# Performance work log

Measured on AMD Instinct MI355X. Metric: run time of the kernel, lower is better.

## Reference

```python
import jax, jax.numpy as jnp
import numpy as np

N_FRAMES = 20000
N_BEADS = 50


def _feature_indices(n_beads):
    # cgnet's get_distance_indices ordering: by pair separation, then start index
    dist = np.array([(i, i + inc) for inc in range(1, n_beads)
                     for i in range(n_beads - inc)], dtype=np.int32)
    ang = np.array([(i, i + 1, i + 2) for i in range(n_beads - 2)], dtype=np.int32)
    dih = np.array([(i, i + 1, i + 2, i + 3) for i in range(n_beads - 3)], dtype=np.int32)
    return dist, ang, dih


def setup_inputs() -> dict:
    key = jax.random.key(0)
    data = jax.random.normal(key, (N_FRAMES, N_BEADS, 3), dtype=jnp.float32) * 3.0
    return {"data": data}


def reference(data):
    # data: [n_frames, n_beads, 3]
    n_beads = data.shape[1]
    dist_inds, ang_inds, dih_inds = _feature_indices(n_beads)

    # --- pairwise distances: ||x_j - x_i|| -> [F, n_dist]
    dvec = data[:, dist_inds[:, 1]] - data[:, dist_inds[:, 0]]
    distances = jnp.linalg.norm(dvec, axis=-1)

    # --- planar angles at middle bead j of (i, j, k) -> [F, n_ang]
    b1 = data[:, ang_inds[:, 0]] - data[:, ang_inds[:, 1]]
    b2 = data[:, ang_inds[:, 2]] - data[:, ang_inds[:, 1]]
    cos_theta = jnp.sum(b1 * b2, axis=-1) / (
        jnp.linalg.norm(b1, axis=-1) * jnp.linalg.norm(b2, axis=-1))
    angles = jnp.arccos(jnp.clip(cos_theta, -1.0, 1.0))

    # --- dihedrals of (i, j, k, l): cross-product plane normals -> cos, sin
    a = data[:, dih_inds[:, 1]] - data[:, dih_inds[:, 0]]
    b = data[:, dih_inds[:, 2]] - data[:, dih_inds[:, 1]]
    c = data[:, dih_inds[:, 3]] - data[:, dih_inds[:, 2]]
    p1 = jnp.cross(a, b)          # normal of plane (i,j,k)
    p2 = jnp.cross(b, c)          # normal of plane (j,k,l)
    n1 = jnp.linalg.norm(p1, axis=-1)
    n2 = jnp.linalg.norm(p2, axis=-1)
    dih_cos = jnp.sum(p1 * p2, axis=-1) / (n1 * n2)
    dih_sin = jnp.sum(jnp.cross(p1, p2) * b, axis=-1) / (
        n1 * n2 * jnp.linalg.norm(b, axis=-1))

    # description_order: Distances, Angles, Dihedral_cosines, Dihedral_sines
    return jnp.concatenate([distances, angles, dih_cos, dih_sin], axis=1)
```

## Files before the change

kernel.cpp:

```cpp
#include <hip/hip_runtime.h>
#include <math.h>

#define N_FRAMES 20000
#define N_BEADS  50
#define N_DIST   1225
#define N_ANG    48
#define N_DIH    47
#define OUT_STRIDE (N_DIST + N_ANG + 2 * N_DIH)

__device__ __forceinline__ int cum_pairs(int inc) {
    return (inc - 1) * 50 - ((inc - 1) * inc) / 2;
}

__global__ __launch_bounds__(256)
void protein_feat_kernel(const float* __restrict__ data, float* __restrict__ out) {
    const int f   = blockIdx.x;
    const int tid = threadIdx.x;

    __shared__ float s[N_BEADS * 3];

    const float* fd = data + (size_t)f * (N_BEADS * 3);
    if (tid < N_BEADS * 3) s[tid] = fd[tid];
    __syncthreads();

    float* fout = out + (size_t)f * OUT_STRIDE;

    for (int p = tid; p < N_DIST; p += 256) {
        float disc = 9801.0f - 8.0f * (float)p;
        int inc = (int)((101.0f - sqrtf(disc)) * 0.5f);
        inc = min(max(inc, 1), 49);
        while (inc < 49 && cum_pairs(inc + 1) <= p) ++inc;
        while (inc > 1  && cum_pairs(inc)     >  p) --inc;
        int i = p - cum_pairs(inc);
        int j = i + inc;

        float dx = s[3 * j + 0] - s[3 * i + 0];
        float dy = s[3 * j + 1] - s[3 * i + 1];
        float dz = s[3 * j + 2] - s[3 * i + 2];
        fout[p] = sqrtf(dx * dx + dy * dy + dz * dz);
    }

    if (tid < N_ANG) {
        int a = tid;
        float b1x = s[3 * a + 0] - s[3 * (a + 1) + 0];
        float b1y = s[3 * a + 1] - s[3 * (a + 1) + 1];
        float b1z = s[3 * a + 2] - s[3 * (a + 1) + 2];
        float b2x = s[3 * (a + 2) + 0] - s[3 * (a + 1) + 0];
        float b2y = s[3 * (a + 2) + 1] - s[3 * (a + 1) + 1];
        float b2z = s[3 * (a + 2) + 2] - s[3 * (a + 1) + 2];
        float dot = b1x * b2x + b1y * b2y + b1z * b2z;
        float n1 = sqrtf(b1x * b1x + b1y * b1y + b1z * b1z);
        float n2 = sqrtf(b2x * b2x + b2y * b2y + b2z * b2z);
        float c = dot / (n1 * n2);
        c = fminf(1.0f, fmaxf(-1.0f, c));
        fout[N_DIST + a] = acosf(c);
    }

    if (tid >= 64 && tid < 64 + N_DIH) {
        int d = tid - 64;
        float ax = s[3 * (d + 1) + 0] - s[3 * d + 0];
        float ay = s[3 * (d + 1) + 1] - s[3 * d + 1];
        float az = s[3 * (d + 1) + 2] - s[3 * d + 2];
        float bx = s[3 * (d + 2) + 0] - s[3 * (d + 1) + 0];
        float by = s[3 * (d + 2) + 1] - s[3 * (d + 1) + 1];
        float bz = s[3 * (d + 2) + 2] - s[3 * (d + 1) + 2];
        float cx = s[3 * (d + 3) + 0] - s[3 * (d + 2) + 0];
        float cy = s[3 * (d + 3) + 1] - s[3 * (d + 2) + 1];
        float cz = s[3 * (d + 3) + 2] - s[3 * (d + 2) + 2];

        float p1x = ay * bz - az * by;
        float p1y = az * bx - ax * bz;
        float p1z = ax * by - ay * bx;
        float p2x = by * cz - bz * cy;
        float p2y = bz * cx - bx * cz;
        float p2z = bx * cy - by * cx;

        float n1 = sqrtf(p1x * p1x + p1y * p1y + p1z * p1z);
        float n2 = sqrtf(p2x * p2x + p2y * p2y + p2z * p2z);
        float nb = sqrtf(bx * bx + by * by + bz * bz);

        float dotp = p1x * p2x + p1y * p2y + p1z * p2z;
        float qx = p1y * p2z - p1z * p2y;
        float qy = p1z * p2x - p1x * p2z;
        float qz = p1x * p2y - p1y * p2x;
        float trip = qx * bx + qy * by + qz * bz;

        float inv12 = 1.0f / (n1 * n2);
        fout[N_DIST + N_ANG + d]          = dotp * inv12;
        fout[N_DIST + N_ANG + N_DIH + d]  = trip * inv12 / nb;
    }
}

extern "C" void kernel_launch(void* const* d_in, const int* in_sizes, int n_in,
                              void* d_out, int out_size, void* d_ws, size_t ws_size,
                              hipStream_t stream) {
    const float* data = (const float*)d_in[0];
    float* out = (float*)d_out;
    protein_feat_kernel<<<N_FRAMES, 256, 0, stream>>>(data, out);
}
```

Before: 149.2 us.

## Process eight frames per block and reuse pair index decoding across frames

Each block now handles eight frames instead of one. It loads all eight with float4 copies into shared memory and decodes the distance pair indices once into registers, then reuses them for every frame. Angle and dihedral work is spread over all threads across the eight frames rather than leaving most threads idle. This cuts per-block launch and setup overhead and the repeated sqrt-based index search, at the cost of fewer blocks (2500) and more registers per thread.

```diff
diff --git a/kernel.cpp b/kernel.cpp
--- a/kernel.cpp
+++ b/kernel.cpp
@@ -7,6 +7,8 @@
 #define N_ANG    48
 #define N_DIH    47
 #define OUT_STRIDE (N_DIST + N_ANG + 2 * N_DIH)
+#define FPB      8
+#define FRAME_F  (N_BEADS * 3)
 
 __device__ __forceinline__ int cum_pairs(int inc) {
     return (inc - 1) * 50 - ((inc - 1) * inc) / 2;
@@ -14,59 +16,83 @@
 
 __global__ __launch_bounds__(256)
 void protein_feat_kernel(const float* __restrict__ data, float* __restrict__ out) {
-    const int f   = blockIdx.x;
     const int tid = threadIdx.x;
+    const int f0  = blockIdx.x * FPB;
 
-    __shared__ float s[N_BEADS * 3];
+    __shared__ __align__(16) float s[FPB * FRAME_F];
 
-    const float* fd = data + (size_t)f * (N_BEADS * 3);
-    if (tid < N_BEADS * 3) s[tid] = fd[tid];
+    {
+        const float4* g4 = (const float4*)(data + (size_t)f0 * FRAME_F);
+        float4* s4 = (float4*)s;
+        for (int x = tid; x < FPB * FRAME_F / 4; x += 256) s4[x] = g4[x];
+    }
     __syncthreads();
 
-    float* fout = out + (size_t)f * OUT_STRIDE;
-
-    for (int p = tid; p < N_DIST; p += 256) {
-        float disc = 9801.0f - 8.0f * (float)p;
-        int inc = (int)((101.0f - sqrtf(disc)) * 0.5f);
-        inc = min(max(inc, 1), 49);
-        while (inc < 49 && cum_pairs(inc + 1) <= p) ++inc;
-        while (inc > 1  && cum_pairs(inc)     >  p) --inc;
-        int i = p - cum_pairs(inc);
-        int j = i + inc;
-
-        float dx = s[3 * j + 0] - s[3 * i + 0];
-        float dy = s[3 * j + 1] - s[3 * i + 1];
-        float dz = s[3 * j + 2] - s[3 * i + 2];
-        fout[p] = sqrtf(dx * dx + dy * dy + dz * dz);
+    int i3[5], j3[5];
+#pragma unroll
+    for (int k = 0; k < 5; ++k) {
+        int p = tid + k * 256;
+        if (p < N_DIST) {
+            float disc = 9801.0f - 8.0f * (float)p;
+            int inc = (int)((101.0f - sqrtf(disc)) * 0.5f);
+            inc = min(max(inc, 1), 49);
+            while (inc < 49 && cum_pairs(inc + 1) <= p) ++inc;
+            while (inc > 1  && cum_pairs(inc)     >  p) --inc;
+            int i = p - cum_pairs(inc);
+            i3[k] = 3 * i;
+            j3[k] = 3 * (i + inc);
+        } else {
+            i3[k] = 0; j3[k] = 0;
+        }
     }
 
-    if (tid < N_ANG) {
-        int a = tid;
-        float b1x = s[3 * a + 0] - s[3 * (a + 1) + 0];
-        float b1y = s[3 * a + 1] - s[3 * (a + 1) + 1];
-        float b1z = s[3 * a + 2] - s[3 * (a + 1) + 2];
-        float b2x = s[3 * (a + 2) + 0] - s[3 * (a + 1) + 0];
-        float b2y = s[3 * (a + 2) + 1] - s[3 * (a + 1) + 1];
-        float b2z = s[3 * (a + 2) + 2] - s[3 * (a + 1) + 2];
+#pragma unroll
+    for (int f = 0; f < FPB; ++f) {
+        const float* sf = s + f * FRAME_F;
+        float* fout = out + (size_t)(f0 + f) * OUT_STRIDE;
+#pragma unroll
+        for (int k = 0; k < 5; ++k) {
+            int p = tid + k * 256;
+            if (p < N_DIST) {
+                float dx = sf[j3[k] + 0] - sf[i3[k] + 0];
+                float dy = sf[j3[k] + 1] - sf[i3[k] + 1];
+                float dz = sf[j3[k] + 2] - sf[i3[k] + 2];
+                fout[p] = sqrtf(dx * dx + dy * dy + dz * dz);
+            }
+        }
+    }
+
+    for (int idx = tid; idx < FPB * N_ANG; idx += 256) {
+        int f = idx / N_ANG;
+        int a = idx - f * N_ANG;
+        const float* sf = s + f * FRAME_F;
+        float b1x = sf[3 * a + 0] - sf[3 * (a + 1) + 0];
+        float b1y = sf[3 * a + 1] - sf[3 * (a + 1) + 1];
+        float b1z = sf[3 * a + 2] - sf[3 * (a + 1) + 2];
+        float b2x = sf[3 * (a + 2) + 0] - sf[3 * (a + 1) + 0];
+        float b2y = sf[3 * (a + 2) + 1] - sf[3 * (a + 1) + 1];
+        float b2z = sf[3 * (a + 2) + 2] - sf[3 * (a + 1) + 2];
         float dot = b1x * b2x + b1y * b2y + b1z * b2z;
         float n1 = sqrtf(b1x * b1x + b1y * b1y + b1z * b1z);
         float n2 = sqrtf(b2x * b2x + b2y * b2y + b2z * b2z);
         float c = dot / (n1 * n2);
         c = fminf(1.0f, fmaxf(-1.0f, c));
-        fout[N_DIST + a] = acosf(c);
+        out[(size_t)(f0 + f) * OUT_STRIDE + N_DIST + a] = acosf(c);
     }
 
-    if (tid >= 64 && tid < 64 + N_DIH) {
-        int d = tid - 64;
-        float ax = s[3 * (d + 1) + 0] - s[3 * d + 0];
-        float ay = s[3 * (d + 1) + 1] - s[3 * d + 1];
-        float az = s[3 * (d + 1) + 2] - s[3 * d + 2];
-        float bx = s[3 * (d + 2) + 0] - s[3 * (d + 1) + 0];
-        float by = s[3 * (d + 2) + 1] - s[3 * (d + 1) + 1];
-        float bz = s[3 * (d + 2) + 2] - s[3 * (d + 1) + 2];
-        float cx = s[3 * (d + 3) + 0] - s[3 * (d + 2) + 0];
-        float cy = s[3 * (d + 3) + 1] - s[3 * (d + 2) + 1];
-        float cz = s[3 * (d + 3) + 2] - s[3 * (d + 2) + 2];
+    for (int idx = tid; idx < FPB * N_DIH; idx += 256) {
+        int f = idx / N_DIH;
+        int d = idx - f * N_DIH;
+        const float* sf = s + f * FRAME_F;
+        float ax = sf[3 * (d + 1) + 0] - sf[3 * d + 0];
+        float ay = sf[3 * (d + 1) + 1] - sf[3 * d + 1];
+        float az = sf[3 * (d + 1) + 2] - sf[3 * d + 2];
+        float bx = sf[3 * (d + 2) + 0] - sf[3 * (d + 1) + 0];
+        float by = sf[3 * (d + 2) + 1] - sf[3 * (d + 1) + 1];
+        float bz = sf[3 * (d + 2) + 2] - sf[3 * (d + 1) + 2];
+        float cx = sf[3 * (d + 3) + 0] - sf[3 * (d + 2) + 0];
+        float cy = sf[3 * (d + 3) + 1] - sf[3 * (d + 2) + 1];
+        float cz = sf[3 * (d + 3) + 2] - sf[3 * (d + 2) + 2];
 
         float p1x = ay * bz - az * by;
         float p1y = az * bx - ax * bz;
@@ -86,8 +112,9 @@
         float trip = qx * bx + qy * by + qz * bz;
 
         float inv12 = 1.0f / (n1 * n2);
-        fout[N_DIST + N_ANG + d]          = dotp * inv12;
-        fout[N_DIST + N_ANG + N_DIH + d]  = trip * inv12 / nb;
+        size_t base = (size_t)(f0 + f) * OUT_STRIDE + N_DIST + N_ANG;
+        out[base + d]         = dotp * inv12;
+        out[base + N_DIH + d] = trip * inv12 / nb;
     }
 }
 
@@ -96,5 +123,5 @@
                               hipStream_t stream) {
     const float* data = (const float*)d_in[0];
     float* out = (float*)d_out;
-    protein_feat_kernel<<<N_FRAMES, 256, 0, stream>>>(data, out);
+    protein_feat_kernel<<<N_FRAMES / FPB, 256, 0, stream>>>(data, out);
 }
```

New measurement: 131.1 us. -12.1%, faster.
